# Performance work log

Hardware: AMD Instinct MI355X
Metric: run time of the kernel (lower is better)

Reference implementation:

```python
import jax, jax.numpy as jnp
import numpy as np

EMBED_DIM = 1024
NUM_HEADS = 16
HEAD_DIM = EMBED_DIM // NUM_HEADS
BATCH = 8
SEQ = 1024


def setup_inputs() -> dict:
    key = jax.random.key(0)
    ks = jax.random.split(key, 10)
    s = 1.0 / np.sqrt(EMBED_DIM)
    x = jax.random.normal(ks[0], (BATCH, SEQ, EMBED_DIM), dtype=jnp.float32)
    mask = jax.random.randint(ks[1], (BATCH, SEQ), 0, 2, dtype=jnp.int32)
    mk = lambda k: (jax.random.normal(k, (EMBED_DIM, EMBED_DIM), dtype=jnp.float32) * s)
    return {
        "x": x, "mask": mask,
        "Wq": mk(ks[2]), "bq": jnp.zeros((EMBED_DIM,), jnp.float32),
        "Wk": mk(ks[3]), "bk": jnp.zeros((EMBED_DIM,), jnp.float32),
        "Wv": mk(ks[4]), "bv": jnp.zeros((EMBED_DIM,), jnp.float32),
        "Wo": mk(ks[5]), "bo": jnp.zeros((EMBED_DIM,), jnp.float32),
    }


def _split_heads(t):
    # (B, S, E) -> (B, H, S, D)
    B, S, _ = t.shape
    return t.reshape(B, S, NUM_HEADS, HEAD_DIM).transpose(0, 2, 1, 3)


def reference(x, mask, Wq, bq, Wk, bk, Wv, bv, Wo, bo):
    B, S, E = x.shape
    # torch Linear: y = x @ W.T + b, weight shape (out, in)
    Q = _split_heads(jnp.einsum('bse,oe->bso', x, Wq) + bq)
    K = _split_heads(jnp.einsum('bse,oe->bso', x, Wk) + bk)
    V = _split_heads(jnp.einsum('bse,oe->bso', x, Wv) + bv)
    scores = jnp.einsum('bhqd,bhkd->bhqk', Q, K) / np.sqrt(HEAD_DIM)
    scores = jnp.clip(scores, -50.0, 50.0)
    m = (mask == 0)[:, None, None, :]  # (B,1,1,S)
    scores = jnp.where(m, jnp.float32(-1e9), scores)
    scores = jnp.where(jnp.isfinite(scores), scores, jnp.zeros_like(scores))
    aw = jax.nn.softmax(scores, axis=-1)
    aw = jnp.where(jnp.isfinite(aw), aw, jnp.zeros_like(aw))
    aw = aw / (aw.sum(axis=-1, keepdims=True) + 1e-10)
    # dropout is identity in eval mode
    attended = jnp.einsum('bhqk,bhkd->bhqd', aw, V)
    attended = attended.transpose(0, 2, 1, 3).reshape(B, S, E)
    output = jnp.einsum('bse,oe->bso', attended, Wo) + bo
    return (output, aw)
```

## Files before the change

### kernel.cpp

```cpp
#include <hip/hip_runtime.h>
#include <stdint.h>

typedef _Float16 f16x8 __attribute__((ext_vector_type(8)));
typedef float    f32x4 __attribute__((ext_vector_type(4)));

#define SEQL 1024
#define EMB  1024
#define NH   16
#define HD   64
#define BATCH 8
#define QKVN 3072

__device__ __forceinline__ void gll16(const void* g, void* l) {
  __builtin_amdgcn_global_load_lds(
      (const __attribute__((address_space(1))) unsigned int*)(uintptr_t)g,
      (__attribute__((address_space(3))) unsigned int*)(uintptr_t)l, 16, 0, 0);
}

__device__ __forceinline__ void cvt8(const float* __restrict__ in,
                                     _Float16* __restrict__ out, int i) {
  const float4* p = (const float4*)in;
  float4 a = p[2 * i], b = p[2 * i + 1];
  f16x8 o;
  o[0] = (_Float16)a.x; o[1] = (_Float16)a.y; o[2] = (_Float16)a.z; o[3] = (_Float16)a.w;
  o[4] = (_Float16)b.x; o[5] = (_Float16)b.y; o[6] = (_Float16)b.z; o[7] = (_Float16)b.w;
  ((f16x8*)out)[i] = o;
}

__global__ __launch_bounds__(256) void k_prep(const float* __restrict__ x,
                                              const float* __restrict__ Wq,
                                              const float* __restrict__ Wk,
                                              const float* __restrict__ Wv,
                                              const float* __restrict__ Wo,
                                              const float* __restrict__ bq,
                                              const float* __restrict__ bk,
                                              const float* __restrict__ bv,
                                              _Float16* __restrict__ x16,
                                              _Float16* __restrict__ Wqkv16,
                                              _Float16* __restrict__ Wo16,
                                              float* __restrict__ bqkv) {
  const int bid = blockIdx.x, tid = threadIdx.x;
  if (bid < 4096) {
    cvt8(x, x16, bid * 256 + tid);
  } else if (bid < 4608) {
    cvt8(Wq, Wqkv16, (bid - 4096) * 256 + tid);
  } else if (bid < 5120) {
    cvt8(Wk, Wqkv16 + (size_t)EMB * EMB, (bid - 4608) * 256 + tid);
  } else if (bid < 5632) {
    cvt8(Wv, Wqkv16 + (size_t)2 * EMB * EMB, (bid - 5120) * 256 + tid);
  } else if (bid < 6144) {
    cvt8(Wo, Wo16, (bid - 5632) * 256 + tid);
  } else {
    int i = (bid - 6144) * 256 + tid;
    float v = (i < 1024) ? bq[i] : (i < 2048 ? bk[i - 1024] : bv[i - 2048]);
    bqkv[i] = v;
  }
}

template <int OUT_F16>
__global__ __launch_bounds__(256) void k_gemm_nt(const _Float16* __restrict__ A,
                                                 const _Float16* __restrict__ B,
                                                 const float* __restrict__ bias,
                                                 void* __restrict__ Cv,
                                                 int M, int N, int K) {
  __shared__ __align__(16) _Float16 As[128 * 32];
  __shared__ __align__(16) _Float16 Bs[128 * 32];
  const int nb = N >> 7;
  const int bm = (int)blockIdx.x / nb, bn = (int)blockIdx.x % nb;
  const int m0 = bm << 7, n0 = bn << 7;
  const int tid = threadIdx.x;
  const int wave = tid >> 6, lane = tid & 63, quad = lane >> 4, l16 = lane & 15;
  const int wm = (wave & 1) << 6, wn = (wave >> 1) << 6;

  f32x4 acc[4][4] = {};

  const int c0 = tid, c1 = tid + 256;
  const int row0 = c0 >> 2, ko0 = (c0 & 3) << 3;
  const int row1 = c1 >> 2, ko1 = (c1 & 3) << 3;
  const _Float16* a0 = A + (size_t)(m0 + row0) * K + ko0;
  const _Float16* a1 = A + (size_t)(m0 + row1) * K + ko1;
  const _Float16* b0 = B + (size_t)(n0 + row0) * K + ko0;
  const _Float16* b1 = B + (size_t)(n0 + row1) * K + ko1;

  for (int k0 = 0; k0 < K; k0 += 32) {
    __syncthreads();
    gll16(a0 + k0, As + (size_t)c0 * 8);
    gll16(a1 + k0, As + (size_t)c1 * 8);
    gll16(b0 + k0, Bs + (size_t)c0 * 8);
    gll16(b1 + k0, Bs + (size_t)c1 * 8);
    __syncthreads();

    f16x8 af[4], bf[4];
#pragma unroll
    for (int i = 0; i < 4; ++i)
      af[i] = *(const f16x8*)(As + ((wm + (i << 4) + l16) << 5) + (quad << 3));
#pragma unroll
    for (int i = 0; i < 4; ++i)
      bf[i] = *(const f16x8*)(Bs + ((wn + (i << 4) + l16) << 5) + (quad << 3));
#pragma unroll
    for (int i = 0; i < 4; ++i)
#pragma unroll
      for (int j = 0; j < 4; ++j)
        acc[i][j] = __builtin_amdgcn_mfma_f32_16x16x32_f16(af[i], bf[j], acc[i][j], 0, 0, 0);
  }

#pragma unroll
  for (int j = 0; j < 4; ++j) {
    int col = n0 + wn + (j << 4) + l16;
    float bb = bias[col];
#pragma unroll
    for (int i = 0; i < 4; ++i) {
      int rowb = m0 + wm + (i << 4) + (quad << 2);
#pragma unroll
      for (int r = 0; r < 4; ++r) {
        float v = acc[i][j][r] + bb;
        if (OUT_F16)
          ((_Float16*)Cv)[(size_t)(rowb + r) * N + col] = (_Float16)v;
        else
          ((float*)Cv)[(size_t)(rowb + r) * N + col] = v;
      }
    }
  }
}

__global__ __launch_bounds__(256) void k_transpose_v(const _Float16* __restrict__ QKV,
                                                     _Float16* __restrict__ Vt) {
  int tid = blockIdx.x * 256 + threadIdx.x;
  int d = tid & 63;
  int s0 = ((tid >> 6) & 127) << 3;
  int h = (tid >> 13) & 15;
  int b = tid >> 17;
  const _Float16* src = QKV + ((size_t)(b * SEQL + s0)) * QKVN + 2048 + h * HD + d;
  f16x8 t;
#pragma unroll
  for (int j = 0; j < 8; ++j) t[j] = src[(size_t)j * QKVN];
  *(f16x8*)(Vt + ((size_t)((b * NH + h) * HD + d)) * SEQL + s0) = t;
}

#define PPAD 272
#define OPAD 68

__device__ __forceinline__ void stage_v(const _Float16* __restrict__ Vme,
                                        _Float16* __restrict__ dst, int c) {
#pragma unroll
  for (int it = 0; it < 8; ++it)
    gll16(Vme + (size_t)it * 8 * SEQL + (size_t)c * 256, dst + (size_t)it * 2048);
}

__global__ __launch_bounds__(256) void k_attn_fused(const _Float16* __restrict__ QKV,
                                                    const _Float16* __restrict__ Vt,
                                                    const int* __restrict__ mask,
                                                    float* __restrict__ aw,
                                                    _Float16* __restrict__ att) {
  __shared__ __align__(16) _Float16 ubuf[16384];
  __shared__ __align__(16) _Float16 pbuf[4][16 * PPAD];
  __shared__ float sm[4][16], sl[4][16];

  const int qt = blockIdx.x, h = blockIdx.y, b = blockIdx.z;
  const int tid = threadIdx.x;
  const int wave = tid >> 6, lane = tid & 63, quad = lane >> 4, l16 = lane & 15;

  const _Float16* Qbase =
      QKV + ((size_t)(b * SEQL + qt * 16 + l16)) * QKVN + h * HD + quad * 8;
  f16x8 qf0 = *(const f16x8*)(Qbase);
  f16x8 qf1 = *(const f16x8*)(Qbase + 32);

  float p[16][4];
  float mr[4], lr[4];
#pragma unroll
  for (int r = 0; r < 4; ++r) mr[r] = -3.0e38f;

  const int* mrow = mask + b * SEQL;

  const _Float16* Kg = QKV + (size_t)b * SEQL * QKVN + 1024 + h * HD;
  const int krow = tid >> 3;
  const int kdch = (tid & 7) ^ (krow & 7);
  const _Float16* Kme = Kg + (size_t)krow * QKVN + kdch * 8;
  const _Float16* Vg = Vt + ((size_t)(b * NH + h)) * HD * SEQL;
  const int vrow = tid >> 5;
  const int vsch = (tid & 31) ^ (vrow & 7);
  const _Float16* Vme = Vg + (size_t)vrow * SEQL + vsch * 8;
  _Float16* kdst = ubuf + (size_t)tid * 8;

  for (int c = 0; c < 4; ++c) {
    if (c) __syncthreads();
#pragma unroll
    for (int it = 0; it < 8; ++it)
      gll16(Kme + (size_t)(c * 256 + it * 32) * QKVN, kdst + (size_t)it * 2048);
    __syncthreads();
#pragma unroll
    for (int ctw = 0; ctw < 4; ++ctw) {
      int sloc = wave * 64 + ctw * 16 + l16;
      int ch0 = sloc * 8 + (quad ^ (sloc & 7));
      f16x8 kf0 = *(const f16x8*)(ubuf + (size_t)ch0 * 8);
      f16x8 kf1 = *(const f16x8*)(ubuf + (size_t)(ch0 ^ 4) * 8);
      f32x4 acc = {};
      acc = __builtin_amdgcn_mfma_f32_16x16x32_f16(qf0, kf0, acc, 0, 0, 0);
      acc = __builtin_amdgcn_mfma_f32_16x16x32_f16(qf1, kf1, acc, 0, 0, 0);
      int col = c * 256 + sloc;
      bool mk = (mrow[col] == 0);
      int pidx = c * 4 + ctw;
#pragma unroll
      for (int r = 0; r < 4; ++r) {
        float s = acc[r] * 0.125f;
        s = fminf(fmaxf(s, -50.f), 50.f);
        if (mk) s = -1.0e9f;
        p[pidx][r] = s;
        mr[r] = fmaxf(mr[r], s);
      }
    }
  }

#pragma unroll
  for (int r = 0; r < 4; ++r) {
    float m = mr[r];
    m = fmaxf(m, __shfl_xor(m, 1, 16));
    m = fmaxf(m, __shfl_xor(m, 2, 16));
    m = fmaxf(m, __shfl_xor(m, 4, 16));
    m = fmaxf(m, __shfl_xor(m, 8, 16));
    mr[r] = m;
  }
#pragma unroll
  for (int r = 0; r < 4; ++r) lr[r] = 0.f;
#pragma unroll
  for (int pidx = 0; pidx < 16; ++pidx) {
#pragma unroll
    for (int r = 0; r < 4; ++r) {
      float e = __expf(p[pidx][r] - mr[r]);
      p[pidx][r] = e;
      lr[r] += e;
    }
  }
#pragma unroll
  for (int r = 0; r < 4; ++r) {
    float l = lr[r];
    l += __shfl_xor(l, 1, 16);
    l += __shfl_xor(l, 2, 16);
    l += __shfl_xor(l, 4, 16);
    l += __shfl_xor(l, 8, 16);
    lr[r] = l;
  }
  if (l16 == 0) {
#pragma unroll
    for (int r = 0; r < 4; ++r) {
      sm[wave][quad * 4 + r] = mr[r];
      sl[wave][quad * 4 + r] = lr[r];
    }
  }
  __syncthreads();

  stage_v(Vme, kdst, 0);

  float f[4];
#pragma unroll
  for (int r = 0; r < 4; ++r) {
    int row = quad * 4 + r;
    float M = fmaxf(fmaxf(sm[0][row], sm[1][row]), fmaxf(sm[2][row], sm[3][row]));
    float L = sl[0][row] * __expf(sm[0][row] - M) + sl[1][row] * __expf(sm[1][row] - M) +
              sl[2][row] * __expf(sm[2][row] - M) + sl[3][row] * __expf(sm[3][row] - M);
    f[r] = __expf(mr[r] - M) / L;
  }

  float* awb = aw + (((size_t)(b * NH + h)) * SEQL + qt * 16) * SEQL;
  _Float16* pw = pbuf[wave];
#pragma unroll
  for (int pidx = 0; pidx < 16; ++pidx) {
    int col = ((pidx >> 2) << 8) + (wave << 6) + ((pidx & 3) << 4) + l16;
#pragma unroll
    for (int r = 0; r < 4; ++r) {
      float v = p[pidx][r] * f[r];
      awb[(size_t)(quad * 4 + r) * SEQL + col] = v;
      pw[(quad * 4 + r) * PPAD + pidx * 16 + l16] = (_Float16)v;
    }
  }

  f32x4 opv[4] = {};
  for (int c = 0; c < 4; ++c) {
    __syncthreads();
#pragma unroll
    for (int ks = 0; ks < 2; ++ks) {
      int klocal = c * 64 + ks * 32;
      f16x8 af = *(const f16x8*)(pw + l16 * PPAD + klocal + quad * 8);
#pragma unroll
      for (int nt = 0; nt < 4; ++nt) {
        int d = nt * 16 + l16;
        int sch = wave * 8 + ks * 4 + quad;
        int ch = d * 32 + (sch ^ (d & 7));
        f16x8 bf = *(const f16x8*)(ubuf + (size_t)ch * 8);
        opv[nt] = __builtin_amdgcn_mfma_f32_16x16x32_f16(af, bf, opv[nt], 0, 0, 0);
      }
    }
    if (c < 3) {
      __syncthreads();
      stage_v(Vme, kdst, c + 1);
    }
  }
  __syncthreads();

  float* ob = (float*)ubuf;
#pragma unroll
  for (int nt = 0; nt < 4; ++nt)
#pragma unroll
    for (int r = 0; r < 4; ++r)
      ob[(wave * 16 + quad * 4 + r) * OPAD + nt * 16 + l16] = opv[nt][r];
  __syncthreads();

  {
    int col = tid & 63;
    int r0 = tid >> 6;
#pragma unroll
    for (int i = 0; i < 4; ++i) {
      int row = r0 + i * 4;
      float o = ob[row * OPAD + col] + ob[(16 + row) * OPAD + col] +
                ob[(32 + row) * OPAD + col] + ob[(48 + row) * OPAD + col];
      att[((size_t)(b * SEQL + qt * 16 + row)) * EMB + h * HD + col] = (_Float16)o;
    }
  }
}

extern "C" void kernel_launch(void* const* d_in, const int* in_sizes, int n_in,
                              void* d_out, int out_size, void* d_ws, size_t ws_size,
                              hipStream_t stream) {
  const float* x  = (const float*)d_in[0];
  const int* mask = (const int*)d_in[1];
  const float* Wq = (const float*)d_in[2];
  const float* bq = (const float*)d_in[3];
  const float* Wk = (const float*)d_in[4];
  const float* bk = (const float*)d_in[5];
  const float* Wv = (const float*)d_in[6];
  const float* bv = (const float*)d_in[7];
  const float* Wo = (const float*)d_in[8];
  const float* bo = (const float*)d_in[9];

  float* out = (float*)d_out;
  float* aw = out + (size_t)BATCH * SEQL * EMB;

  char* ws = (char*)d_ws;
  _Float16* x16    = (_Float16*)(ws);
  _Float16* Wqkv16 = (_Float16*)(ws + ((size_t)16 << 20));
  _Float16* Wo16   = (_Float16*)(ws + ((size_t)22 << 20));
  float*    bqkv   = (float*)   (ws + ((size_t)24 << 20));
  _Float16* QKV16  = (_Float16*)(ws + ((size_t)25 << 20));
  _Float16* Vt16   = (_Float16*)(ws + ((size_t)73 << 20));
  _Float16* att16  = (_Float16*)(ws + ((size_t)89 << 20));

  const int M = BATCH * SEQL;

  k_prep<<<6156, 256, 0, stream>>>(x, Wq, Wk, Wv, Wo, bq, bk, bv,
                                   x16, Wqkv16, Wo16, bqkv);

  k_gemm_nt<1><<<(M / 128) * (QKVN / 128), 256, 0, stream>>>(x16, Wqkv16, bqkv, QKV16,
                                                             M, QKVN, EMB);

  k_transpose_v<<<4096, 256, 0, stream>>>(QKV16, Vt16);

  k_attn_fused<<<dim3(SEQL / 16, NH, BATCH), 256, 0, stream>>>(QKV16, Vt16, mask, aw, att16);

  k_gemm_nt<0><<<(M / 128) * (EMB / 128), 256, 0, stream>>>(att16, Wo16, bo, out,
                                                            M, EMB, EMB);
}
```

Measured before the change: 912.8 us.

## Shrink attention LDS footprint and read V directly from global memory

The K staging buffer is halved, with K processed in eight 128-key chunks instead of four 256-key chunks. The per-wave P buffer is halved by writing and consuming probabilities in two halves. V is no longer staged through LDS with block-wide syncs; each wave loads V fragments directly from global memory into the MFMA operands, and launch bounds request 4 blocks per CU. The aim is higher occupancy and fewer barriers, at the cost of uncoalesced or redundant global V reads and more K-loop iterations.

```diff
diff --git a/kernel.cpp b/kernel.cpp
--- a/kernel.cpp
+++ b/kernel.cpp
@@ -137,23 +137,16 @@
   *(f16x8*)(Vt + ((size_t)((b * NH + h) * HD + d)) * SEQL + s0) = t;
 }
 
-#define PPAD 272
+#define PPAD2 136
 #define OPAD 68
 
-__device__ __forceinline__ void stage_v(const _Float16* __restrict__ Vme,
-                                        _Float16* __restrict__ dst, int c) {
-#pragma unroll
-  for (int it = 0; it < 8; ++it)
-    gll16(Vme + (size_t)it * 8 * SEQL + (size_t)c * 256, dst + (size_t)it * 2048);
-}
-
-__global__ __launch_bounds__(256) void k_attn_fused(const _Float16* __restrict__ QKV,
-                                                    const _Float16* __restrict__ Vt,
-                                                    const int* __restrict__ mask,
-                                                    float* __restrict__ aw,
-                                                    _Float16* __restrict__ att) {
-  __shared__ __align__(16) _Float16 ubuf[16384];
-  __shared__ __align__(16) _Float16 pbuf[4][16 * PPAD];
+__global__ __launch_bounds__(256, 4) void k_attn_fused(const _Float16* __restrict__ QKV,
+                                                       const _Float16* __restrict__ Vt,
+                                                       const int* __restrict__ mask,
+                                                       float* __restrict__ aw,
+                                                       _Float16* __restrict__ att) {
+  __shared__ __align__(16) _Float16 kbuf[8192];
+  __shared__ __align__(16) char pob[4][4352];
   __shared__ float sm[4][16], sl[4][16];
 
   const int qt = blockIdx.x, h = blockIdx.y, b = blockIdx.z;
@@ -176,30 +169,26 @@
   const int krow = tid >> 3;
   const int kdch = (tid & 7) ^ (krow & 7);
   const _Float16* Kme = Kg + (size_t)krow * QKVN + kdch * 8;
-  const _Float16* Vg = Vt + ((size_t)(b * NH + h)) * HD * SEQL;
-  const int vrow = tid >> 5;
-  const int vsch = (tid & 31) ^ (vrow & 7);
-  const _Float16* Vme = Vg + (size_t)vrow * SEQL + vsch * 8;
-  _Float16* kdst = ubuf + (size_t)tid * 8;
-
-  for (int c = 0; c < 4; ++c) {
+  _Float16* kdst = kbuf + (size_t)tid * 8;
+
+  for (int c = 0; c < 8; ++c) {
     if (c) __syncthreads();
 #pragma unroll
-    for (int it = 0; it < 8; ++it)
-      gll16(Kme + (size_t)(c * 256 + it * 32) * QKVN, kdst + (size_t)it * 2048);
+    for (int g = 0; g < 4; ++g)
+      gll16(Kme + (size_t)(c * 128 + g * 32) * QKVN, kdst + (size_t)g * 2048);
     __syncthreads();
 #pragma unroll
-    for (int ctw = 0; ctw < 4; ++ctw) {
-      int sloc = wave * 64 + ctw * 16 + l16;
+    for (int ctw = 0; ctw < 2; ++ctw) {
+      int sloc = wave * 32 + ctw * 16 + l16;
       int ch0 = sloc * 8 + (quad ^ (sloc & 7));
-      f16x8 kf0 = *(const f16x8*)(ubuf + (size_t)ch0 * 8);
-      f16x8 kf1 = *(const f16x8*)(ubuf + (size_t)(ch0 ^ 4) * 8);
+      f16x8 kf0 = *(const f16x8*)(kbuf + (size_t)ch0 * 8);
+      f16x8 kf1 = *(const f16x8*)(kbuf + (size_t)(ch0 ^ 4) * 8);
       f32x4 acc = {};
       acc = __builtin_amdgcn_mfma_f32_16x16x32_f16(qf0, kf0, acc, 0, 0, 0);
       acc = __builtin_amdgcn_mfma_f32_16x16x32_f16(qf1, kf1, acc, 0, 0, 0);
-      int col = c * 256 + sloc;
+      int col = c * 128 + sloc;
       bool mk = (mrow[col] == 0);
-      int pidx = c * 4 + ctw;
+      int pidx = c * 2 + ctw;
 #pragma unroll
       for (int r = 0; r < 4; ++r) {
         float s = acc[r] * 0.125f;
@@ -249,8 +238,6 @@
   }
   __syncthreads();
 
-  stage_v(Vme, kdst, 0);
-
   float f[4];
 #pragma unroll
   for (int r = 0; r < 4; ++r) {
@@ -262,42 +249,35 @@
   }
 
   float* awb = aw + (((size_t)(b * NH + h)) * SEQL + qt * 16) * SEQL;
-  _Float16* pw = pbuf[wave];
-#pragma unroll
-  for (int pidx = 0; pidx < 16; ++pidx) {
-    int col = ((pidx >> 2) << 8) + (wave << 6) + ((pidx & 3) << 4) + l16;
-#pragma unroll
-    for (int r = 0; r < 4; ++r) {
-      float v = p[pidx][r] * f[r];
-      awb[(size_t)(quad * 4 + r) * SEQL + col] = v;
-      pw[(quad * 4 + r) * PPAD + pidx * 16 + l16] = (_Float16)v;
-    }
-  }
-
+  _Float16* pw = (_Float16*)pob[wave];
+  const _Float16* vtb = Vt + ((size_t)(b * NH + h)) * HD * SEQL;
   f32x4 opv[4] = {};
-  for (int c = 0; c < 4; ++c) {
-    __syncthreads();
-#pragma unroll
-    for (int ks = 0; ks < 2; ++ks) {
-      int klocal = c * 64 + ks * 32;
-      f16x8 af = *(const f16x8*)(pw + l16 * PPAD + klocal + quad * 8);
+#pragma unroll
+  for (int hf = 0; hf < 2; ++hf) {
+#pragma unroll
+    for (int pl = 0; pl < 8; ++pl) {
+      int pidx = hf * 8 + pl;
+      int col = ((pidx >> 1) << 7) + (wave << 5) + ((pidx & 1) << 4) + l16;
+#pragma unroll
+      for (int r = 0; r < 4; ++r) {
+        float v = p[pidx][r] * f[r];
+        awb[(size_t)(quad * 4 + r) * SEQL + col] = v;
+        pw[(quad * 4 + r) * PPAD2 + pl * 16 + l16] = (_Float16)v;
+      }
+    }
+#pragma unroll
+    for (int j = 0; j < 4; ++j) {
+      f16x8 af = *(const f16x8*)(pw + l16 * PPAD2 + j * 32 + quad * 8);
+      int sbase = ((hf * 4 + j) << 7) + (wave << 5) + (quad << 3);
 #pragma unroll
       for (int nt = 0; nt < 4; ++nt) {
-        int d = nt * 16 + l16;
-        int sch = wave * 8 + ks * 4 + quad;
-        int ch = d * 32 + (sch ^ (d & 7));
-        f16x8 bf = *(const f16x8*)(ubuf + (size_t)ch * 8);
+        f16x8 bf = *(const f16x8*)(vtb + (size_t)(nt * 16 + l16) * SEQL + sbase);
         opv[nt] = __builtin_amdgcn_mfma_f32_16x16x32_f16(af, bf, opv[nt], 0, 0, 0);
       }
     }
-    if (c < 3) {
-      __syncthreads();
-      stage_v(Vme, kdst, c + 1);
-    }
-  }
-  __syncthreads();
-
-  float* ob = (float*)ubuf;
+  }
+
+  float* ob = (float*)&pob[0][0];
 #pragma unroll
   for (int nt = 0; nt < 4; ++nt)
 #pragma unroll
```

Result: no change. 912.7 us (-0.0%).
